# Kernel optimization log

Hardware: AMD Instinct MI355X
Metric: run time of the kernel (lower is better)

Reference implementation:

```python
import jax, jax.numpy as jnp
import numpy as np

B, N, V, H = 8, 2048, 256, 1024
EPS = 1e-5
NEG = -1e9


def _layernorm(x, g, b):
    m = jnp.mean(x, axis=-1, keepdims=True)
    v = jnp.mean((x - m) ** 2, axis=-1, keepdims=True)
    return (x - m) / jnp.sqrt(v + EPS) * g + b


def setup_inputs() -> dict:
    key = jax.random.key(0)
    ks = jax.random.split(key, 10)
    tril = jnp.tril(jnp.ones((N, N), jnp.float32))
    return {
        "h": jax.random.normal(ks[0], (B, N, V), jnp.float32),
        "mask_one": tril,                      # keep causal entries
        "mask_zero": NEG * (1.0 - tril),       # -inf-ish above diagonal
        "ln_attn_g": jnp.ones((V,), jnp.float32),
        "ln_attn_b": jnp.zeros((V,), jnp.float32),
        "ln_mlp_g": jnp.ones((V,), jnp.float32),
        "ln_mlp_b": jnp.zeros((V,), jnp.float32),
        "wv": jax.random.normal(ks[1], (V,), jnp.float32),
        "wv_bos": jax.random.normal(ks[2], (V,), jnp.float32),
        "wo_w": jax.random.normal(ks[3], (V, V), jnp.float32) / np.sqrt(V),
        "qk_bos": jax.random.normal(ks[4], (V,), jnp.float32),
        "qk_previous": jax.random.normal(ks[5], (V,), jnp.float32),
        "qk_direction": jnp.ones((V,), jnp.float32),  # middel_layer=False, frozen
        "w1": jax.random.normal(ks[6], (H, V), jnp.float32) / np.sqrt(V),
        "w2": jax.random.normal(ks[7], (V, H), jnp.float32) / np.sqrt(H),
    }


def reference(h, mask_one, mask_zero, ln_attn_g, ln_attn_b, ln_mlp_g, ln_mlp_b,
              wv, wv_bos, wo_w, qk_bos, qk_previous, qk_direction, w1, w2):
    b, n, v = h.shape
    # mask blends LayerNorm only into row 0 (BOS position)
    attn_input = h.at[:, 0, :].set(_layernorm(h[:, 0, :], ln_attn_g, ln_attn_b))
    # value states: diag(wv) on positions 1.., wo(wv_bos) at position 0
    values = attn_input[:, 1:, :] * wv                      # [B, N-1, V]
    v_bos = wo_w @ wv_bos                                   # Linear(bias=False)
    values = jnp.concatenate(
        [jnp.broadcast_to(v_bos, (b, 1, v)), values], axis=1)  # [B, N, V]
    # sparse QK logits: column 0 term + sub-diagonal term, densified then masked
    col0 = (attn_input @ qk_bos) * (attn_input[:, 0, :] @ qk_direction)[:, None]  # [B, N]
    d = attn_input @ qk_previous                            # [B, N]
    qk = jnp.zeros((b, n, n), h.dtype).at[:, :, 0].add(col0)
    idx = jnp.arange(1, n)
    qk = qk.at[:, idx, idx - 1].add(d[:, 1:])               # row r, col r-1 = d[:, r]
    qk = qk * mask_one + mask_zero
    attn_out = jax.nn.softmax(qk, axis=-1) @ values         # [B, N, V]
    # FFN branch with its own BOS-only LayerNorm blend
    mlp_input = h.at[:, 0, :].set(_layernorm(h[:, 0, :], ln_mlp_g, ln_mlp_b))
    mlp_out = jax.nn.relu(mlp_input @ w1.T) @ w2.T          # [B, N, V]
    return attn_out + mlp_out
```

## Files before the change

### kernel.cpp

```cpp
#include <hip/hip_runtime.h>
#include <hip/hip_bf16.h>

#define BB 8
#define NN 2048
#define VV 256
#define HH 1024
#define CHK 64
#define RPC 32
constexpr float EPS = 1e-5f;

typedef __attribute__((ext_vector_type(4))) float floatx4;
typedef __attribute__((ext_vector_type(8))) short short8;

__device__ __forceinline__ void load_lds16(const void* g, void* l) {
    __builtin_amdgcn_global_load_lds((const __attribute__((address_space(1))) void*)g,
                                     (__attribute__((address_space(3))) void*)l, 16, 0, 0);
}

__global__ void prep_kernel(const float* __restrict__ h,
                            const float* __restrict__ g_attn, const float* __restrict__ b_attn,
                            const float* __restrict__ g_mlp,  const float* __restrict__ b_mlp,
                            const float* __restrict__ qk_dir,
                            const float* __restrict__ wo_w,  const float* __restrict__ wv_bos,
                            float* __restrict__ attn_row0, float* __restrict__ mlp_row0,
                            float* __restrict__ v_bos, float* __restrict__ sum0)
{
    int t = threadIdx.x;
    __shared__ float red[VV];
    if (blockIdx.x < BB) {
        int b = blockIdx.x;
        float x = h[(size_t)b * NN * VV + t];
        red[t] = x; __syncthreads();
        for (int s = 128; s > 0; s >>= 1) { if (t < s) red[t] += red[t + s]; __syncthreads(); }
        float m = red[0] * (1.0f / VV); __syncthreads();
        float xc = x - m;
        red[t] = xc * xc; __syncthreads();
        for (int s = 128; s > 0; s >>= 1) { if (t < s) red[t] += red[t + s]; __syncthreads(); }
        float var = red[0] * (1.0f / VV); __syncthreads();
        float inv = 1.0f / sqrtf(var + EPS);
        float an = xc * inv * g_attn[t] + b_attn[t];
        float mn = xc * inv * g_mlp[t] + b_mlp[t];
        attn_row0[b * VV + t] = an;
        mlp_row0[b * VV + t]  = mn;
        red[t] = an * qk_dir[t]; __syncthreads();
        for (int s = 128; s > 0; s >>= 1) { if (t < s) red[t] += red[t + s]; __syncthreads(); }
        if (t == 0) sum0[b] = red[0];
    } else {
        const float4* wp = reinterpret_cast<const float4*>(wo_w + (size_t)t * VV);
        const float4* vp = reinterpret_cast<const float4*>(wv_bos);
        float acc = 0.f;
        for (int j = 0; j < VV / 4; ++j) {
            float4 a = wp[j], b = vp[j];
            acc += a.x * b.x + a.y * b.y + a.z * b.z + a.w * b.w;
        }
        v_bos[t] = acc;
    }
}

__global__ __launch_bounds__(256) void scan_qkw_cvt_kernel(
    const float* __restrict__ h, const float* __restrict__ mlp_row0,
    const float* __restrict__ wv,
    const float* __restrict__ qk_bos, const float* __restrict__ qk_prev,
    const float* __restrict__ sum0,
    short* __restrict__ Xb,
    float* __restrict__ w0, float* __restrict__ wprev, float* __restrict__ wz,
    float* __restrict__ chunkSum)
{
    __shared__ float lds[4][VV];
    int wave = threadIdx.x >> 6, lane = threadIdx.x & 63;
    int b = blockIdx.x / CHK, c = blockIdx.x % CHK;
    int r0 = c * RPC + wave * 8;
    float4 wv4 = reinterpret_cast<const float4*>(wv)[lane];
    float4 qb4 = reinterpret_cast<const float4*>(qk_bos)[lane];
    float4 qp4 = reinterpret_cast<const float4*>(qk_prev)[lane];
    float s0b = sum0[b];
    float4 vsum = {0.f, 0.f, 0.f, 0.f};
#pragma unroll
    for (int rr = 0; rr < 8; ++rr) {
        int r = r0 + rr;
        size_t base = ((size_t)b * NN + r) * VV;
        float4 x = *reinterpret_cast<const float4*>(h + base + lane * 4);
        float4 xs = x;
        if (r == 0) xs = *reinterpret_cast<const float4*>(mlp_row0 + b * VV + lane * 4);
        __hip_bfloat16 c0 = __float2bfloat16(xs.x), c1 = __float2bfloat16(xs.y),
                       c2 = __float2bfloat16(xs.z), c3 = __float2bfloat16(xs.w);
        short4 pk;
        pk.x = *reinterpret_cast<short*>(&c0);
        pk.y = *reinterpret_cast<short*>(&c1);
        pk.z = *reinterpret_cast<short*>(&c2);
        pk.w = *reinterpret_cast<short*>(&c3);
        *reinterpret_cast<short4*>(Xb + base + lane * 4) = pk;
        if (r != 0) {
            vsum.x += x.x * wv4.x; vsum.y += x.y * wv4.y;
            vsum.z += x.z * wv4.z; vsum.w += x.w * wv4.w;
        }
        float s1 = x.x * qb4.x + x.y * qb4.y + x.z * qb4.z + x.w * qb4.w;
        float s2 = x.x * qp4.x + x.y * qp4.y + x.z * qp4.z + x.w * qp4.w;
        for (int off = 32; off > 0; off >>= 1) {
            s1 += __shfl_down(s1, off);
            s2 += __shfl_down(s2, off);
        }
        if (lane == 0) {
            int gid = b * NN + r;
            float W0, WP, WZ;
            if (r == 0) { W0 = 1.f; WP = 0.f; WZ = 0.f; }
            else if (r == 1) {
                float a = s1 * s0b + s2;
                float m = fmaxf(a, 0.f);
                float ea = expf(a - m), ez = expf(-m);
                float Z = ea + ez;
                W0 = ea / Z; WZ = ez / Z; WP = WZ;
            } else {
                float a = s1 * s0b;
                float m = fmaxf(fmaxf(a, s2), 0.f);
                float ea = expf(a - m), ed = expf(s2 - m), ez = expf(-m);
                float Z = ea + ed + (float)(r - 1) * ez;
                W0 = ea / Z; WP = ed / Z; WZ = ez / Z;
            }
            w0[gid] = W0; wprev[gid] = WP; wz[gid] = WZ;
        }
    }
    reinterpret_cast<float4*>(lds[wave])[lane] = vsum;
    __syncthreads();
    int v = threadIdx.x;
    chunkSum[((size_t)b * CHK + c) * VV + v] = lds[0][v] + lds[1][v] + lds[2][v] + lds[3][v];
}

__global__ void chunkscan_kernel(float* __restrict__ chunkSum)
{
    int b = blockIdx.x, v = threadIdx.x;
    float run = 0.f;
    for (int c = 0; c < CHK; ++c) {
        int idx = (b * CHK + c) * VV + v;
        float t = chunkSum[idx];
        chunkSum[idx] = run;
        run += t;
    }
}

__global__ void attn_kernel(const float* __restrict__ h, const float* __restrict__ wv,
                            const float* __restrict__ v_bos,
                            const float* __restrict__ w0, const float* __restrict__ wprev,
                            const float* __restrict__ wz, const float* __restrict__ chunkSum,
                            float* __restrict__ out)
{
    int b = blockIdx.x / CHK, c = blockIdx.x % CHK;
    int v = threadIdx.x;
    float wvv = wv[v], vb = v_bos[v];
    float S = chunkSum[(b * CHK + c) * VV + v];
    int r0 = c * RPC;
    float prev = (r0 == 0) ? 0.f : h[((size_t)b * NN + r0 - 1) * VV + v] * wvv;
    for (int r = r0; r < r0 + RPC; ++r) {
        size_t idx = ((size_t)b * NN + r) * VV + v;
        float o;
        if (r == 0) {
            o = vb;
            prev = 0.f;
        } else {
            float val = h[idx] * wvv;
            S += val;
            int wi = b * NN + r;
            o = w0[wi] * vb + (wprev[wi] - wz[wi]) * prev + wz[wi] * S;
            prev = val;
        }
        out[idx] = o;
    }
}

__global__ void cvt_w_kernel(const float* __restrict__ w1, const float* __restrict__ w2,
                             __hip_bfloat16* __restrict__ w1b, __hip_bfloat16* __restrict__ w2b)
{
    int i = (blockIdx.x * blockDim.x + threadIdx.x) * 4;
    const float* src;
    __hip_bfloat16* dst;
    if (i < HH * VV) { src = w1 + i; dst = w1b + i; }
    else             { src = w2 + (i - HH * VV); dst = w2b + (i - HH * VV); }
    float4 x = *reinterpret_cast<const float4*>(src);
    dst[0] = __float2bfloat16(x.x);
    dst[1] = __float2bfloat16(x.y);
    dst[2] = __float2bfloat16(x.z);
    dst[3] = __float2bfloat16(x.w);
}

__global__ __launch_bounds__(512) void mlp_fused(const short* __restrict__ Xb,
                                                 const short* __restrict__ w1b,
                                                 const short* __restrict__ w2b,
                                                 float* __restrict__ out)
{
    __shared__ __align__(16) short sX[64 * 256];
    __shared__ __align__(16) short sW1[64 * 256];
    __shared__ __align__(16) short sW2[256 * 64];
    __shared__ __align__(16) short sY[64 * 64];
    int wave = threadIdx.x >> 6, lane = threadIdx.x & 63;
    int wm = wave >> 2, wn = wave & 3;
    int m0 = blockIdx.x * 64;
    int ra = lane & 15, q = lane >> 4;

    floatx4 oacc[2][4];
#pragma unroll
    for (int i = 0; i < 2; ++i)
#pragma unroll
        for (int j = 0; j < 4; ++j) oacc[i][j] = floatx4{0.f, 0.f, 0.f, 0.f};

    {
        int rp = lane >> 5, segp = lane & 31;
#pragma unroll
        for (int i = 0; i < 4; ++i) {
            int L = wave * 4 + i;
            int row = L * 2 + rp;
            int g = segp ^ (row & 7);
            load_lds16(Xb + (size_t)(m0 + row) * 256 + g * 8, sX + L * 512);
        }
    }

    for (int hc = 0; hc < 16; ++hc) {
        __syncthreads();
        {
            int rp = lane >> 5, segp = lane & 31;
#pragma unroll
            for (int i = 0; i < 4; ++i) {
                int L = wave * 4 + i;
                int row = L * 2 + rp;
                int g = segp ^ (row & 7);
                load_lds16(w1b + (size_t)(hc * 64 + row) * 256 + g * 8, sW1 + L * 512);
            }
            int rp2 = lane >> 3, segp2 = lane & 7;
#pragma unroll
            for (int i = 0; i < 4; ++i) {
                int L = wave * 4 + i;
                int row = L * 8 + rp2;
                int g = segp2 ^ (row & 7);
                load_lds16(w2b + (size_t)row * 1024 + hc * 64 + g * 8, sW2 + L * 512);
            }
        }
        __syncthreads();

        floatx4 yacc[2];
        yacc[0] = floatx4{0.f, 0.f, 0.f, 0.f};
        yacc[1] = floatx4{0.f, 0.f, 0.f, 0.f};
#pragma unroll
        for (int kk = 0; kk < 8; ++kk) {
            int g = kk * 4 + q;
            int n = wn * 16 + ra;
            short8 bfr = *reinterpret_cast<const short8*>(sW1 + n * 256 + ((g ^ (n & 7)) * 8));
#pragma unroll
            for (int i = 0; i < 2; ++i) {
                int m = wm * 32 + i * 16 + ra;
                short8 a = *reinterpret_cast<const short8*>(sX + m * 256 + ((g ^ (m & 7)) * 8));
                yacc[i] = __builtin_amdgcn_mfma_f32_16x16x32_bf16(a, bfr, yacc[i], 0, 0, 0);
            }
        }

#pragma unroll
        for (int i = 0; i < 2; ++i) {
#pragma unroll
            for (int reg = 0; reg < 4; ++reg) {
                int me = wm * 32 + i * 16 + q * 4 + reg;
                int ke = wn * 16 + ra;
                float v = fmaxf(yacc[i][reg], 0.f);
                __hip_bfloat16 hb = __float2bfloat16(v);
                sY[me * 64 + (((ke >> 3) ^ (me & 7)) * 8) + (ke & 7)] =
                    *reinterpret_cast<short*>(&hb);
            }
        }
        __syncthreads();

#pragma unroll
        for (int kk2 = 0; kk2 < 2; ++kk2) {
            int g = kk2 * 4 + q;
            short8 a2[2];
#pragma unroll
            for (int i = 0; i < 2; ++i) {
                int m = wm * 32 + i * 16 + ra;
                a2[i] = *reinterpret_cast<const short8*>(sY + m * 64 + ((g ^ (m & 7)) * 8));
            }
#pragma unroll
            for (int j = 0; j < 4; ++j) {
                int n = wn * 64 + j * 16 + ra;
                short8 b2 = *reinterpret_cast<const short8*>(sW2 + n * 64 + ((g ^ (n & 7)) * 8));
#pragma unroll
                for (int i = 0; i < 2; ++i)
                    oacc[i][j] = __builtin_amdgcn_mfma_f32_16x16x32_bf16(a2[i], b2, oacc[i][j], 0, 0, 0);
            }
        }
    }

#pragma unroll
    for (int i = 0; i < 2; ++i) {
#pragma unroll
        for (int j = 0; j < 4; ++j) {
#pragma unroll
            for (int reg = 0; reg < 4; ++reg) {
                int row = m0 + wm * 32 + i * 16 + q * 4 + reg;
                int col = wn * 64 + j * 16 + ra;
                out[(size_t)row * VV + col] += oacc[i][j][reg];
            }
        }
    }
}

extern "C" void kernel_launch(void* const* d_in, const int* in_sizes, int n_in,
                              void* d_out, int out_size, void* d_ws, size_t ws_size,
                              hipStream_t stream)
{
    const float* h        = (const float*)d_in[0];
    const float* ln_attn_g = (const float*)d_in[3];
    const float* ln_attn_b = (const float*)d_in[4];
    const float* ln_mlp_g  = (const float*)d_in[5];
    const float* ln_mlp_b  = (const float*)d_in[6];
    const float* wv        = (const float*)d_in[7];
    const float* wv_bos    = (const float*)d_in[8];
    const float* wo_w      = (const float*)d_in[9];
    const float* qk_bos    = (const float*)d_in[10];
    const float* qk_prev   = (const float*)d_in[11];
    const float* qk_dir    = (const float*)d_in[12];
    const float* w1        = (const float*)d_in[13];
    const float* w2        = (const float*)d_in[14];
    float* out = (float*)d_out;

    float* attn_row0 = (float*)d_ws;
    float* mlp_row0  = attn_row0 + BB * VV;
    float* v_bos     = mlp_row0 + BB * VV;
    float* sum0      = v_bos + VV;
    float* w0        = sum0 + 8;
    float* wprev     = w0 + BB * NN;
    float* wzz       = wprev + BB * NN;
    float* chunkSum  = wzz + BB * NN;
    short* Xb            = (short*)(chunkSum + BB * CHK * VV);
    __hip_bfloat16* w1b  = (__hip_bfloat16*)(Xb + (size_t)BB * NN * VV);
    __hip_bfloat16* w2b  = w1b + HH * VV;

    prep_kernel<<<BB + 1, 256, 0, stream>>>(h, ln_attn_g, ln_attn_b, ln_mlp_g, ln_mlp_b,
                                            qk_dir, wo_w, wv_bos,
                                            attn_row0, mlp_row0, v_bos, sum0);
    cvt_w_kernel<<<(2 * HH * VV / 4) / 256, 256, 0, stream>>>(w1, w2, w1b, w2b);
    scan_qkw_cvt_kernel<<<BB * CHK, 256, 0, stream>>>(h, mlp_row0, wv, qk_bos, qk_prev,
                                                      sum0, Xb, w0, wprev, wzz, chunkSum);
    chunkscan_kernel<<<BB, 256, 0, stream>>>(chunkSum);
    attn_kernel<<<BB * CHK, 256, 0, stream>>>(h, wv, v_bos, w0, wprev, wzz, chunkSum, out);
    mlp_fused<<<256, 512, 0, stream>>>(Xb, (const short*)w1b, (const short*)w2b, out);
}
```

Measured before the change: 182.3 us.

## Restructure MLP kernel with register-resident X and wider hidden chunks; read bf16 in attention

The fused MLP kernel now holds the 64-row X tile in registers, processes 128-wide hidden chunks with 4 waves instead of 16 chunks of 64 with 8 waves, and drops the XOR swizzle in LDS. The attention kernel reads the bf16 copy of h instead of fp32 and handles two columns per thread. The chunk scan is unrolled through registers, and the scan kernel's value sums are switched to bf16-rounded inputs so they match the attention path. These changes aim to cut global traffic and LDS/sync overhead. In exchange the attention values lose precision, and the unswizzled LDS reads may cause bank conflicts.

```diff
diff --git a/kernel.cpp b/kernel.cpp
--- a/kernel.cpp
+++ b/kernel.cpp
@@ -15,6 +15,10 @@
 __device__ __forceinline__ void load_lds16(const void* g, void* l) {
     __builtin_amdgcn_global_load_lds((const __attribute__((address_space(1))) void*)g,
                                      (__attribute__((address_space(3))) void*)l, 16, 0, 0);
+}
+__device__ __forceinline__ float bf16s_to_f(short s) {
+    unsigned u = ((unsigned)(unsigned short)s) << 16;
+    return __builtin_bit_cast(float, u);
 }
 
 __global__ void prep_kernel(const float* __restrict__ h,
@@ -91,8 +95,8 @@
         pk.w = *reinterpret_cast<short*>(&c3);
         *reinterpret_cast<short4*>(Xb + base + lane * 4) = pk;
         if (r != 0) {
-            vsum.x += x.x * wv4.x; vsum.y += x.y * wv4.y;
-            vsum.z += x.z * wv4.z; vsum.w += x.w * wv4.w;
+            vsum.x += bf16s_to_f(pk.x) * wv4.x; vsum.y += bf16s_to_f(pk.y) * wv4.y;
+            vsum.z += bf16s_to_f(pk.z) * wv4.z; vsum.w += bf16s_to_f(pk.w) * wv4.w;
         }
         float s1 = x.x * qb4.x + x.y * qb4.y + x.z * qb4.z + x.w * qb4.w;
         float s2 = x.x * qp4.x + x.y * qp4.y + x.z * qp4.z + x.w * qp4.w;
@@ -129,41 +133,52 @@
 __global__ void chunkscan_kernel(float* __restrict__ chunkSum)
 {
     int b = blockIdx.x, v = threadIdx.x;
+    float vals[CHK];
+#pragma unroll
+    for (int c = 0; c < CHK; ++c) vals[c] = chunkSum[(b * CHK + c) * VV + v];
     float run = 0.f;
-    for (int c = 0; c < CHK; ++c) {
-        int idx = (b * CHK + c) * VV + v;
-        float t = chunkSum[idx];
-        chunkSum[idx] = run;
-        run += t;
-    }
-}
-
-__global__ void attn_kernel(const float* __restrict__ h, const float* __restrict__ wv,
-                            const float* __restrict__ v_bos,
-                            const float* __restrict__ w0, const float* __restrict__ wprev,
-                            const float* __restrict__ wz, const float* __restrict__ chunkSum,
-                            float* __restrict__ out)
+#pragma unroll
+    for (int c = 0; c < CHK; ++c) { float t = vals[c]; vals[c] = run; run += t; }
+#pragma unroll
+    for (int c = 0; c < CHK; ++c) chunkSum[(b * CHK + c) * VV + v] = vals[c];
+}
+
+__global__ __launch_bounds__(128) void attn_kernel(
+    const short* __restrict__ Xb, const float* __restrict__ wv,
+    const float* __restrict__ v_bos,
+    const float* __restrict__ w0, const float* __restrict__ wprev,
+    const float* __restrict__ wz, const float* __restrict__ chunkSum,
+    float* __restrict__ out)
 {
     int b = blockIdx.x / CHK, c = blockIdx.x % CHK;
-    int v = threadIdx.x;
-    float wvv = wv[v], vb = v_bos[v];
-    float S = chunkSum[(b * CHK + c) * VV + v];
+    int v = threadIdx.x * 2;
+    float2 wv2 = *reinterpret_cast<const float2*>(wv + v);
+    float2 vb2 = *reinterpret_cast<const float2*>(v_bos + v);
+    float2 S = *reinterpret_cast<const float2*>(chunkSum + (b * CHK + c) * VV + v);
     int r0 = c * RPC;
-    float prev = (r0 == 0) ? 0.f : h[((size_t)b * NN + r0 - 1) * VV + v] * wvv;
+    float2 prev = {0.f, 0.f};
+    if (r0 > 0) {
+        short2 p = *reinterpret_cast<const short2*>(Xb + ((size_t)b * NN + r0 - 1) * VV + v);
+        prev.x = bf16s_to_f(p.x) * wv2.x; prev.y = bf16s_to_f(p.y) * wv2.y;
+    }
     for (int r = r0; r < r0 + RPC; ++r) {
         size_t idx = ((size_t)b * NN + r) * VV + v;
-        float o;
+        float2 o;
         if (r == 0) {
-            o = vb;
-            prev = 0.f;
+            o = vb2;
+            prev.x = 0.f; prev.y = 0.f;
         } else {
-            float val = h[idx] * wvv;
-            S += val;
+            short2 xv = *reinterpret_cast<const short2*>(Xb + idx);
+            float2 val;
+            val.x = bf16s_to_f(xv.x) * wv2.x; val.y = bf16s_to_f(xv.y) * wv2.y;
+            S.x += val.x; S.y += val.y;
             int wi = b * NN + r;
-            o = w0[wi] * vb + (wprev[wi] - wz[wi]) * prev + wz[wi] * S;
+            float W0 = w0[wi], WD = wprev[wi] - wz[wi], WZ = wz[wi];
+            o.x = W0 * vb2.x + WD * prev.x + WZ * S.x;
+            o.y = W0 * vb2.y + WD * prev.y + WZ * S.y;
             prev = val;
         }
-        out[idx] = o;
+        *reinterpret_cast<float2*>(out + idx) = o;
     }
 }
 
@@ -182,121 +197,106 @@
     dst[3] = __float2bfloat16(x.w);
 }
 
-__global__ __launch_bounds__(512) void mlp_fused(const short* __restrict__ Xb,
-                                                 const short* __restrict__ w1b,
-                                                 const short* __restrict__ w2b,
-                                                 float* __restrict__ out)
-{
-    __shared__ __align__(16) short sX[64 * 256];
-    __shared__ __align__(16) short sW1[64 * 256];
-    __shared__ __align__(16) short sW2[256 * 64];
-    __shared__ __align__(16) short sY[64 * 64];
+__global__ __launch_bounds__(256) void mlp_fused2(const short* __restrict__ Xb,
+                                                  const short* __restrict__ w1b,
+                                                  const short* __restrict__ w2b,
+                                                  float* __restrict__ out)
+{
+    __shared__ __align__(16) short sW1[128 * 256];
+    __shared__ __align__(16) short sW2[256 * 128];
+    __shared__ __align__(16) short sY[64 * 128];
     int wave = threadIdx.x >> 6, lane = threadIdx.x & 63;
-    int wm = wave >> 2, wn = wave & 3;
+    int ra = lane & 15, q = lane >> 4;
     int m0 = blockIdx.x * 64;
-    int ra = lane & 15, q = lane >> 4;
-
-    floatx4 oacc[2][4];
-#pragma unroll
-    for (int i = 0; i < 2; ++i)
+
+    short8 xf[8][4];
+#pragma unroll
+    for (int ks = 0; ks < 8; ++ks)
+#pragma unroll
+        for (int i = 0; i < 4; ++i)
+            xf[ks][i] = *reinterpret_cast<const short8*>(
+                Xb + (size_t)(m0 + i * 16 + ra) * VV + ks * 32 + q * 8);
+
+    floatx4 oacc[4][4];
+#pragma unroll
+    for (int i = 0; i < 4; ++i)
 #pragma unroll
         for (int j = 0; j < 4; ++j) oacc[i][j] = floatx4{0.f, 0.f, 0.f, 0.f};
 
-    {
-        int rp = lane >> 5, segp = lane & 31;
-#pragma unroll
-        for (int i = 0; i < 4; ++i) {
-            int L = wave * 4 + i;
-            int row = L * 2 + rp;
-            int g = segp ^ (row & 7);
-            load_lds16(Xb + (size_t)(m0 + row) * 256 + g * 8, sX + L * 512);
-        }
-    }
-
-    for (int hc = 0; hc < 16; ++hc) {
+    auto stage = [&](int hc) {
+#pragma unroll
+        for (int it = 0; it < 16; ++it) {
+            int g = wave * 16 + it;
+            load_lds16(w1b + ((size_t)(hc * 128 + g * 2) * VV) + lane * 8, sW1 + g * 512);
+        }
+#pragma unroll
+        for (int it = 0; it < 16; ++it) {
+            int v4 = wave * 64 + it * 4 + (lane >> 4);
+            short8 t = *reinterpret_cast<const short8*>(
+                w2b + (size_t)v4 * HH + hc * 128 + (lane & 15) * 8);
+            *reinterpret_cast<short8*>(sW2 + v4 * 128 + (lane & 15) * 8) = t;
+        }
+    };
+
+    stage(0);
+    for (int hc = 0; hc < 8; ++hc) {
         __syncthreads();
-        {
-            int rp = lane >> 5, segp = lane & 31;
-#pragma unroll
-            for (int i = 0; i < 4; ++i) {
-                int L = wave * 4 + i;
-                int row = L * 2 + rp;
-                int g = segp ^ (row & 7);
-                load_lds16(w1b + (size_t)(hc * 64 + row) * 256 + g * 8, sW1 + L * 512);
+        floatx4 yacc[4][2];
+#pragma unroll
+        for (int i = 0; i < 4; ++i) { yacc[i][0] = floatx4{0,0,0,0}; yacc[i][1] = floatx4{0,0,0,0}; }
+#pragma unroll
+        for (int ks = 0; ks < 8; ++ks) {
+#pragma unroll
+            for (int j = 0; j < 2; ++j) {
+                int n = wave * 32 + j * 16 + ra;
+                short8 bfr = *reinterpret_cast<const short8*>(sW1 + n * 256 + ks * 32 + q * 8);
+#pragma unroll
+                for (int i = 0; i < 4; ++i)
+                    yacc[i][j] = __builtin_amdgcn_mfma_f32_16x16x32_bf16(xf[ks][i], bfr, yacc[i][j], 0, 0, 0);
             }
-            int rp2 = lane >> 3, segp2 = lane & 7;
-#pragma unroll
-            for (int i = 0; i < 4; ++i) {
-                int L = wave * 4 + i;
-                int row = L * 8 + rp2;
-                int g = segp2 ^ (row & 7);
-                load_lds16(w2b + (size_t)row * 1024 + hc * 64 + g * 8, sW2 + L * 512);
-            }
-        }
+        }
+#pragma unroll
+        for (int i = 0; i < 4; ++i)
+#pragma unroll
+            for (int j = 0; j < 2; ++j)
+#pragma unroll
+                for (int reg = 0; reg < 4; ++reg) {
+                    int row = i * 16 + q * 4 + reg;
+                    int col = wave * 32 + j * 16 + ra;
+                    __hip_bfloat16 hb = __float2bfloat16(fmaxf(yacc[i][j][reg], 0.f));
+                    sY[row * 128 + col] = *reinterpret_cast<short*>(&hb);
+                }
         __syncthreads();
 
-        floatx4 yacc[2];
-        yacc[0] = floatx4{0.f, 0.f, 0.f, 0.f};
-        yacc[1] = floatx4{0.f, 0.f, 0.f, 0.f};
-#pragma unroll
-        for (int kk = 0; kk < 8; ++kk) {
-            int g = kk * 4 + q;
-            int n = wn * 16 + ra;
-            short8 bfr = *reinterpret_cast<const short8*>(sW1 + n * 256 + ((g ^ (n & 7)) * 8));
-#pragma unroll
-            for (int i = 0; i < 2; ++i) {
-                int m = wm * 32 + i * 16 + ra;
-                short8 a = *reinterpret_cast<const short8*>(sX + m * 256 + ((g ^ (m & 7)) * 8));
-                yacc[i] = __builtin_amdgcn_mfma_f32_16x16x32_bf16(a, bfr, yacc[i], 0, 0, 0);
-            }
-        }
-
-#pragma unroll
-        for (int i = 0; i < 2; ++i) {
-#pragma unroll
-            for (int reg = 0; reg < 4; ++reg) {
-                int me = wm * 32 + i * 16 + q * 4 + reg;
-                int ke = wn * 16 + ra;
-                float v = fmaxf(yacc[i][reg], 0.f);
-                __hip_bfloat16 hb = __float2bfloat16(v);
-                sY[me * 64 + (((ke >> 3) ^ (me & 7)) * 8) + (ke & 7)] =
-                    *reinterpret_cast<short*>(&hb);
-            }
-        }
-        __syncthreads();
-
-#pragma unroll
-        for (int kk2 = 0; kk2 < 2; ++kk2) {
-            int g = kk2 * 4 + q;
-            short8 a2[2];
-#pragma unroll
-            for (int i = 0; i < 2; ++i) {
-                int m = wm * 32 + i * 16 + ra;
-                a2[i] = *reinterpret_cast<const short8*>(sY + m * 64 + ((g ^ (m & 7)) * 8));
-            }
+#pragma unroll
+        for (int kk = 0; kk < 4; ++kk) {
+            short8 a2[4];
+#pragma unroll
+            for (int i = 0; i < 4; ++i)
+                a2[i] = *reinterpret_cast<const short8*>(sY + (i * 16 + ra) * 128 + kk * 32 + q * 8);
 #pragma unroll
             for (int j = 0; j < 4; ++j) {
-                int n = wn * 64 + j * 16 + ra;
-                short8 b2 = *reinterpret_cast<const short8*>(sW2 + n * 64 + ((g ^ (n & 7)) * 8));
-#pragma unroll
-                for (int i = 0; i < 2; ++i)
+                int n = wave * 64 + j * 16 + ra;
+                short8 b2 = *reinterpret_cast<const short8*>(sW2 + n * 128 + kk * 32 + q * 8);
+#pragma unroll
+                for (int i = 0; i < 4; ++i)
                     oacc[i][j] = __builtin_amdgcn_mfma_f32_16x16x32_bf16(a2[i], b2, oacc[i][j], 0, 0, 0);
             }
         }
-    }
-
-#pragma unroll
-    for (int i = 0; i < 2; ++i) {
-#pragma unroll
-        for (int j = 0; j < 4; ++j) {
+        __syncthreads();
+        if (hc < 7) stage(hc + 1);
+    }
+
+#pragma unroll
+    for (int i = 0; i < 4; ++i)
+#pragma unroll
+        for (int j = 0; j < 4; ++j)
 #pragma unroll
             for (int reg = 0; reg < 4; ++reg) {
-                int row = m0 + wm * 32 + i * 16 + q * 4 + reg;
-                int col = wn * 64 + j * 16 + ra;
+                int row = m0 + i * 16 + q * 4 + reg;
+                int col = wave * 64 + j * 16 + ra;
                 out[(size_t)row * VV + col] += oacc[i][j][reg];
             }
-        }
-    }
 }
 
 extern "C" void kernel_launch(void* const* d_in, const int* in_sizes, int n_in,
@@ -337,6 +337,6 @@
     scan_qkw_cvt_kernel<<<BB * CHK, 256, 0, stream>>>(h, mlp_row0, wv, qk_bos, qk_prev,
                                                       sum0, Xb, w0, wprev, wzz, chunkSum);
     chunkscan_kernel<<<BB, 256, 0, stream>>>(chunkSum);
-    attn_kernel<<<BB * CHK, 256, 0, stream>>>(h, wv, v_bos, w0, wprev, wzz, chunkSum, out);
-    mlp_fused<<<256, 512, 0, stream>>>(Xb, (const short*)w1b, (const short*)w2b, out);
-}
+    attn_kernel<<<BB * CHK, 128, 0, stream>>>(Xb, wv, v_bos, w0, wprev, wzz, chunkSum, out);
+    mlp_fused2<<<256, 256, 0, stream>>>(Xb, (const short*)w1b, (const short*)w2b, out);
+}
```

Measured after the change: 190.8 us. 4.7% more time.
